# Optimization experiments

Measured on AMD Instinct MI355X. Metric: run time of the kernel, lower is better.

Reference implementation:

```python
import jax, jax.numpy as jnp
import numpy as np

DECAY = 0.85          # decay_factor
LAM = 0.5             # lambda_diversity
EPS = 1e-12


def setup_inputs() -> dict:
    key = jax.random.key(0)
    ks = jax.random.split(key, 6)
    N, D = 32768, 512
    return {
        "predictions": jax.random.normal(ks[0], (N,), jnp.float32),
        "target_scores": jax.random.normal(ks[1], (N,), jnp.float32),
        "context_embeddings": jax.random.normal(ks[2], (N, D), jnp.float32),
        "input_embeddings": jax.random.normal(ks[3], (N, D), jnp.float32),
        "dsm_embeddings": jax.random.normal(ks[4], (N, D), jnp.float32),
        "explanation_embeddings": jax.random.normal(ks[5], (N, D), jnp.float32),
        "k": 16,
    }


def reference(predictions, target_scores, context_embeddings, input_embeddings,
              dsm_embeddings, explanation_embeddings, k):
    # relevance probabilities over all N candidates (dim=0 softmax as in torch)
    rel = jax.nn.softmax(predictions.squeeze(), axis=0)

    # L2-normalize once so cos_sim is a plain dot product
    E = explanation_embeddings
    En = E / (jnp.linalg.norm(E, axis=-1, keepdims=True) + EPS)  # [N, D]
    N = En.shape[0]

    # Greedy ERR/MMR relevance-diversity selection of k items:
    #   score_t(i) = decay^t * rel[i] - lambda * max_{j in selected} cos(E_i, E_j)
    # pick argmax over unselected; err_score_t = decay^t * rel[selected_t]
    def step(carry, t):
        mask, max_sim = carry                       # [N] bool, [N] f32
        decay = DECAY ** t.astype(rel.dtype)
        score = decay * rel - LAM * max_sim
        score = jnp.where(mask, -jnp.inf, score)
        idx = jnp.argmax(score)
        err = rel[idx] * decay
        sim_new = En @ En[idx]                      # cos sim of all to new pick
        return (mask.at[idx].set(True),
                jnp.maximum(max_sim, sim_new)), (err, idx)

    init = (jnp.zeros((N,), bool), jnp.zeros((N,), rel.dtype))
    _, (errs, sel) = jax.lax.scan(step, init, jnp.arange(k))

    err_loss = -jnp.sum(errs)

    # mmr_loss = -sum_i max_j cos(E_i, E_j) over selected set (self included,
    # exactly as the original code does with util.cos_sim(...).max())
    S = En[sel]                                    # [k, D]
    sims = S @ S.T                                 # [k, k]
    mmr_loss = -jnp.sum(jnp.max(sims, axis=1))

    return err_loss + LAM * mmr_loss
```

## Files before the change

kernel.cpp:

```cpp
#include <hip/hip_runtime.h>
#include <cmath>


#define DECAYF 0.85f
#define LAMF   0.5f
#define EPSF   1e-12f

constexpr int D    = 512;
constexpr int KMAX = 16;
constexpr int NBLK = 256;
constexpr int TPB  = 512;
constexpr int NW   = TPB / 64;
constexpr int RPW  = 16;
constexpr int RPB  = NW * RPW;

using u32 = unsigned int;
using u64 = unsigned long long;

__device__ inline float wsum(float v) {
#pragma unroll
    for (int o = 32; o > 0; o >>= 1) v += __shfl_xor(v, o);
    return v;
}
__device__ inline float wmaxf(float v) {
#pragma unroll
    for (int o = 32; o > 0; o >>= 1) v = fmaxf(v, __shfl_xor(v, o));
    return v;
}
__device__ inline u64 wmax64(u64 v) {
#pragma unroll
    for (int o = 32; o > 0; o >>= 1) {
        u64 w = __shfl_xor(v, o);
        v = (w > v) ? w : v;
    }
    return v;
}
__device__ inline u32 fkey(float f) {
    u32 u = __float_as_uint(f);
    return (u & 0x80000000u) ? ~u : (u | 0x80000000u);
}
__device__ inline u64 poll_slot(u64* p) {
    u64 v = __hip_atomic_load(p, __ATOMIC_RELAXED, __HIP_MEMORY_SCOPE_AGENT);
    while (v == 0ull)
        v = __hip_atomic_load(p, __ATOMIC_RELAXED, __HIP_MEMORY_SCOPE_AGENT);
    return v;
}
__device__ inline void publish(u64* p, u64 v) {
    __hip_atomic_store(p, v, __ATOMIC_RELAXED, __HIP_MEMORY_SCOPE_AGENT);
}

__global__ __launch_bounds__(TPB, 2) void fused_kernel(
        const float* __restrict__ pred,
        const float* __restrict__ E,
        const int*   __restrict__ kptr,
        float* __restrict__ out,
        u64*   __restrict__ sm,
        u64*   __restrict__ part,
        u64*   __restrict__ bcast) {
    const int b = blockIdx.x, tid = threadIdx.x;
    const int wv = tid >> 6, lane = tid & 63;

    __shared__ float pred_s[RPB];
    __shared__ u64   wkey_s[NW];
    __shared__ u64   scan_s[NBLK];
    __shared__ float m_s, S_s;
    __shared__ int   j_s;
    __shared__ int   sel_s[KMAX];
    __shared__ float invsel_s[KMAX];
    __shared__ float rmax_s[KMAX];

    int kk = kptr[0];
    if (kk > KMAX) kk = KMAX;
    if (kk < 0) kk = 0;

    if (tid < RPB) pred_s[tid] = pred[b * RPB + tid];
    __syncthreads();
    if (wv == 0) {
        float p0 = pred_s[lane], p1 = pred_s[lane + 64];
        float mb = wmaxf(fmaxf(p0, p1));
        float sb = wsum(expf(p0 - mb) + expf(p1 - mb));
        if (lane == 0)
            publish(&sm[b], ((u64)__float_as_uint(mb) << 32) | __float_as_uint(sb));
    }
    asm volatile("" ::: "memory");

    const int row0 = b * RPB + wv * RPW;
    float r[RPW][8];
#pragma unroll
    for (int rr = 0; rr < RPW; ++rr) {
        const float4* p = (const float4*)(E + (size_t)(row0 + rr) * D) + 2 * lane;
        float4 a0 = p[0], a1 = p[1];
        r[rr][0] = a0.x; r[rr][1] = a0.y; r[rr][2] = a0.z; r[rr][3] = a0.w;
        r[rr][4] = a1.x; r[rr][5] = a1.y; r[rr][6] = a1.z; r[rr][7] = a1.w;
        float ss = 0.f;
#pragma unroll
        for (int e = 0; e < 8; ++e) ss += r[rr][e] * r[rr][e];
        ss = wsum(ss);
        float inv = 1.f / (sqrtf(ss) + EPSF);
#pragma unroll
        for (int e = 0; e < 8; ++e) r[rr][e] *= inv;
        asm volatile("" : "+v"(r[rr][0]), "+v"(r[rr][1]), "+v"(r[rr][2]), "+v"(r[rr][3]),
                          "+v"(r[rr][4]), "+v"(r[rr][5]), "+v"(r[rr][6]), "+v"(r[rr][7]));
    }

    if (tid < NBLK) scan_s[tid] = poll_slot(&sm[tid]);
    __syncthreads();
    if (wv == 0) {
        u64 v0 = scan_s[lane], v1 = scan_s[lane + 64],
            v2 = scan_s[lane + 128], v3 = scan_s[lane + 192];
        float m0 = __uint_as_float((u32)(v0 >> 32)), m1 = __uint_as_float((u32)(v1 >> 32));
        float m2 = __uint_as_float((u32)(v2 >> 32)), m3 = __uint_as_float((u32)(v3 >> 32));
        float M = wmaxf(fmaxf(fmaxf(m0, m1), fmaxf(m2, m3)));
        float acc = __uint_as_float((u32)(v0 & 0xFFFFFFFFull)) * expf(m0 - M)
                  + __uint_as_float((u32)(v1 & 0xFFFFFFFFull)) * expf(m1 - M)
                  + __uint_as_float((u32)(v2 & 0xFFFFFFFFull)) * expf(m2 - M)
                  + __uint_as_float((u32)(v3 & 0xFFFFFFFFull)) * expf(m3 - M);
        acc = wsum(acc);
        if (lane == 0) { m_s = M; S_s = acc; }
    }
    __syncthreads();
    const float M    = m_s;
    const float Sinv = 1.f / S_s;

    float rel_r[RPW], msim_r[RPW];
#pragma unroll
    for (int rr = 0; rr < RPW; ++rr) {
        rel_r[rr]  = expf(pred_s[wv * RPW + rr] - M) * Sinv;
        msim_r[rr] = 0.f;
    }

    int jprev = -1;
    for (int t = 0; t < KMAX; ++t) {
        if (t >= kk) break;
        const float decay = powf(DECAYF, (float)t);
        if (t > 0) {
            const float4* pj = (const float4*)(E + (size_t)jprev * D) + 2 * lane;
            float4 b0 = pj[0], b1 = pj[1];
            float bj[8] = {b0.x, b0.y, b0.z, b0.w, b1.x, b1.y, b1.z, b1.w};
            float ss = 0.f;
#pragma unroll
            for (int e = 0; e < 8; ++e) ss += bj[e] * bj[e];
            ss = wsum(ss);
            const float js = 1.f / (sqrtf(ss) + EPSF);
#pragma unroll
            for (int e = 0; e < 8; ++e) bj[e] *= js;
#pragma unroll
            for (int rr = 0; rr < RPW; ++rr) {
                float d = 0.f;
#pragma unroll
                for (int e = 0; e < 8; ++e) d += r[rr][e] * bj[e];
                d = wsum(d);
                msim_r[rr] = (row0 + rr == jprev) ? INFINITY
                                                  : fmaxf(msim_r[rr], d);
            }
        }
        u64 best = 0ull;
#pragma unroll
        for (int rr = 0; rr < RPW; ++rr) {
            const float sc = decay * rel_r[rr] - LAMF * msim_r[rr];
            const u64 key = ((u64)fkey(sc) << 32) | (u32)~(u32)(row0 + rr);
            best = (key > best) ? key : best;
        }
        if (lane == 0) wkey_s[wv] = best;
        __syncthreads();
        if (wv == 0) {
            u64 v = (lane < NW) ? wkey_s[lane] : 0ull;
            v = wmax64(v);
            if (lane == 0) publish(&part[t * NBLK + b], v);
        }
        if (b == 0) {
            if (tid < NBLK) scan_s[tid] = poll_slot(&part[t * NBLK + tid]);
            __syncthreads();
            if (wv == 0) {
                u64 v = scan_s[lane];
                u64 w = scan_s[lane + 64];  v = (w > v) ? w : v;
                w = scan_s[lane + 128];     v = (w > v) ? w : v;
                w = scan_s[lane + 192];     v = (w > v) ? w : v;
                v = wmax64(v);
                if (lane == 0) publish(&bcast[t], v);
            }
        }
        if (tid == 0) {
            const int j = (int)~(u32)(poll_slot(&bcast[t]) & 0xFFFFFFFFull);
            j_s = j;
            sel_s[t] = j;
        }
        __syncthreads();
        jprev = j_s;
    }

    if (b == 0) {
        for (int ii = wv; ii < kk; ii += NW) {
            const int si = sel_s[ii];
            const float4* pa = (const float4*)(E + (size_t)si * D) + 2 * lane;
            float4 a0 = pa[0], a1 = pa[1];
            float ss = a0.x*a0.x + a0.y*a0.y + a0.z*a0.z + a0.w*a0.w
                     + a1.x*a1.x + a1.y*a1.y + a1.z*a1.z + a1.w*a1.w;
            ss = wsum(ss);
            if (lane == 0) invsel_s[ii] = 1.f / (sqrtf(ss) + EPSF);
        }
        __syncthreads();
        for (int ii = wv; ii < kk; ii += NW) {
            const int si = sel_s[ii];
            const float4* pa = (const float4*)(E + (size_t)si * D) + 2 * lane;
            float4 a0 = pa[0], a1 = pa[1];
            const float ia = invsel_s[ii];
            float av[8] = {a0.x * ia, a0.y * ia, a0.z * ia, a0.w * ia,
                           a1.x * ia, a1.y * ia, a1.z * ia, a1.w * ia};
            float m = -INFINITY;
            for (int jj = 0; jj < kk; ++jj) {
                const float4* pb = (const float4*)(E + (size_t)sel_s[jj] * D) + 2 * lane;
                float4 c0 = pb[0], c1 = pb[1];
                float d = av[0]*c0.x + av[1]*c0.y + av[2]*c0.z + av[3]*c0.w
                        + av[4]*c1.x + av[5]*c1.y + av[6]*c1.z + av[7]*c1.w;
                d = wsum(d);
                m = fmaxf(m, d * invsel_s[jj]);
            }
            if (lane == 0) rmax_s[ii] = m;
        }
        __syncthreads();
        if (tid == 0) {
            float es = 0.f, mm = 0.f;
            for (int t = 0; t < kk; ++t) {
                es += powf(DECAYF, (float)t) * expf(pred[sel_s[t]] - M) * Sinv;
                mm += rmax_s[t];
            }
            out[0] = -es - LAMF * mm;
        }
    }
}

extern "C" void kernel_launch(void* const* d_in, const int* in_sizes, int n_in,
                              void* d_out, int out_size, void* d_ws, size_t ws_size,
                              hipStream_t stream) {
    const float* pred = (const float*)d_in[0];
    const float* E    = (const float*)d_in[5];
    const int*   kptr = (const int*)d_in[6];
    float* out        = (float*)d_out;

    u64* sm    = (u64*)d_ws;
    u64* part  = sm + NBLK;
    u64* bcast = part + KMAX * NBLK;
    hipMemsetAsync(d_ws, 0, (NBLK + KMAX * NBLK + KMAX) * sizeof(u64), stream);

    void* args[] = {(void*)&pred, (void*)&E, (void*)&kptr, (void*)&out,
                    (void*)&sm, (void*)&part, (void*)&bcast};
    hipLaunchCooperativeKernel((const void*)fused_kernel,
                               dim3(NBLK), dim3(TPB), args, 0, stream);
}
```

Before: 156.8 us.

## Replace per-step block barriers with LDS flag polling and widen blocks

Removes the __syncthreads barriers inside the greedy selection loop. Wave 0 instead polls per-step LDS slots for the other waves' keys, does the cross-block reduction (block 0) and the broadcast poll, then publishes the chosen index through an LDS flag that the other waves spin on. Block size doubles to 1024 threads with 8 rows per wave, so each wave keeps fewer rows in registers. An s_sleep is added to the global polling loop to ease memory traffic. The changes add spin-wait risk and alter occupancy and register pressure.

Measured after the change: 161.8 us. 3.2% more time.

```diff
diff --git a/kernel.cpp b/kernel.cpp
--- a/kernel.cpp
+++ b/kernel.cpp
@@ -9,9 +9,9 @@
 constexpr int D    = 512;
 constexpr int KMAX = 16;
 constexpr int NBLK = 256;
-constexpr int TPB  = 512;
+constexpr int TPB  = 1024;
 constexpr int NW   = TPB / 64;
-constexpr int RPW  = 16;
+constexpr int RPW  = 8;
 constexpr int RPB  = NW * RPW;
 
 using u32 = unsigned int;
@@ -41,15 +41,35 @@
 }
 __device__ inline u64 poll_slot(u64* p) {
     u64 v = __hip_atomic_load(p, __ATOMIC_RELAXED, __HIP_MEMORY_SCOPE_AGENT);
-    while (v == 0ull)
+    while (v == 0ull) {
+        __builtin_amdgcn_s_sleep(1);
         v = __hip_atomic_load(p, __ATOMIC_RELAXED, __HIP_MEMORY_SCOPE_AGENT);
+    }
     return v;
 }
 __device__ inline void publish(u64* p, u64 v) {
     __hip_atomic_store(p, v, __ATOMIC_RELAXED, __HIP_MEMORY_SCOPE_AGENT);
 }
-
-__global__ __launch_bounds__(TPB, 2) void fused_kernel(
+__device__ inline u64 lds_poll64(u64* p) {
+    u64 v = __hip_atomic_load(p, __ATOMIC_RELAXED, __HIP_MEMORY_SCOPE_WORKGROUP);
+    while (v == 0ull)
+        v = __hip_atomic_load(p, __ATOMIC_RELAXED, __HIP_MEMORY_SCOPE_WORKGROUP);
+    return v;
+}
+__device__ inline int lds_poll32(int* p) {
+    int v = __hip_atomic_load(p, __ATOMIC_RELAXED, __HIP_MEMORY_SCOPE_WORKGROUP);
+    while (v == 0)
+        v = __hip_atomic_load(p, __ATOMIC_RELAXED, __HIP_MEMORY_SCOPE_WORKGROUP);
+    return v;
+}
+__device__ inline void lds_store64(u64* p, u64 v) {
+    __hip_atomic_store(p, v, __ATOMIC_RELAXED, __HIP_MEMORY_SCOPE_WORKGROUP);
+}
+__device__ inline void lds_store32(int* p, int v) {
+    __hip_atomic_store(p, v, __ATOMIC_RELAXED, __HIP_MEMORY_SCOPE_WORKGROUP);
+}
+
+__global__ __launch_bounds__(TPB, 4) void fused_kernel(
         const float* __restrict__ pred,
         const float* __restrict__ E,
         const int*   __restrict__ kptr,
@@ -61,17 +81,19 @@
     const int wv = tid >> 6, lane = tid & 63;
 
     __shared__ float pred_s[RPB];
-    __shared__ u64   wkey_s[NW];
     __shared__ u64   scan_s[NBLK];
+    __shared__ u64   wkey_s[KMAX][NW];
+    __shared__ int   jslot_s[KMAX];
     __shared__ float m_s, S_s;
-    __shared__ int   j_s;
-    __shared__ int   sel_s[KMAX];
     __shared__ float invsel_s[KMAX];
     __shared__ float rmax_s[KMAX];
 
     int kk = kptr[0];
     if (kk > KMAX) kk = KMAX;
     if (kk < 0) kk = 0;
+
+    if (tid < KMAX) jslot_s[tid] = 0;
+    if (tid < KMAX * NW) ((u64*)wkey_s)[tid] = 0ull;
 
     if (tid < RPB) pred_s[tid] = pred[b * RPB + tid];
     __syncthreads();
@@ -129,12 +151,14 @@
         msim_r[rr] = 0.f;
     }
 
-    int jprev = -1;
+    int j = -1;
     for (int t = 0; t < KMAX; ++t) {
         if (t >= kk) break;
+        if (t > 0 && wv != 0)
+            j = lds_poll32(&jslot_s[t - 1]) - 1;
         const float decay = powf(DECAYF, (float)t);
         if (t > 0) {
-            const float4* pj = (const float4*)(E + (size_t)jprev * D) + 2 * lane;
+            const float4* pj = (const float4*)(E + (size_t)j * D) + 2 * lane;
             float4 b0 = pj[0], b1 = pj[1];
             float bj[8] = {b0.x, b0.y, b0.z, b0.w, b1.x, b1.y, b1.z, b1.w};
             float ss = 0.f;
@@ -150,8 +174,8 @@
 #pragma unroll
                 for (int e = 0; e < 8; ++e) d += r[rr][e] * bj[e];
                 d = wsum(d);
-                msim_r[rr] = (row0 + rr == jprev) ? INFINITY
-                                                  : fmaxf(msim_r[rr], d);
+                msim_r[rr] = (row0 + rr == j) ? INFINITY
+                                              : fmaxf(msim_r[rr], d);
             }
         }
         u64 best = 0ull;
@@ -161,37 +185,36 @@
             const u64 key = ((u64)fkey(sc) << 32) | (u32)~(u32)(row0 + rr);
             best = (key > best) ? key : best;
         }
-        if (lane == 0) wkey_s[wv] = best;
-        __syncthreads();
+        if (lane == 0) lds_store64(&wkey_s[t][wv], best);
+
         if (wv == 0) {
-            u64 v = (lane < NW) ? wkey_s[lane] : 0ull;
+            u64 v = 0ull;
+            if (lane < NW) v = lds_poll64(&wkey_s[t][lane]);
             v = wmax64(v);
             if (lane == 0) publish(&part[t * NBLK + b], v);
-        }
-        if (b == 0) {
-            if (tid < NBLK) scan_s[tid] = poll_slot(&part[t * NBLK + tid]);
-            __syncthreads();
-            if (wv == 0) {
-                u64 v = scan_s[lane];
-                u64 w = scan_s[lane + 64];  v = (w > v) ? w : v;
-                w = scan_s[lane + 128];     v = (w > v) ? w : v;
-                w = scan_s[lane + 192];     v = (w > v) ? w : v;
-                v = wmax64(v);
-                if (lane == 0) publish(&bcast[t], v);
-            }
-        }
-        if (tid == 0) {
-            const int j = (int)~(u32)(poll_slot(&bcast[t]) & 0xFFFFFFFFull);
-            j_s = j;
-            sel_s[t] = j;
-        }
-        __syncthreads();
-        jprev = j_s;
+            if (b == 0) {
+                u64 a0 = poll_slot(&part[t * NBLK + lane]);
+                u64 a1 = poll_slot(&part[t * NBLK + lane + 64]);
+                u64 a2 = poll_slot(&part[t * NBLK + lane + 128]);
+                u64 a3 = poll_slot(&part[t * NBLK + lane + 192]);
+                u64 m = (a1 > a0) ? a1 : a0;
+                m = (a2 > m) ? a2 : m;
+                m = (a3 > m) ? a3 : m;
+                m = wmax64(m);
+                if (lane == 0) publish(&bcast[t], m);
+            }
+            int jj = 0;
+            if (lane == 0) {
+                jj = (int)~(u32)(poll_slot(&bcast[t]) & 0xFFFFFFFFull);
+                lds_store32(&jslot_s[t], jj + 1);
+            }
+            j = __shfl(jj, 0);
+        }
     }
 
     if (b == 0) {
         for (int ii = wv; ii < kk; ii += NW) {
-            const int si = sel_s[ii];
+            const int si = lds_poll32(&jslot_s[ii]) - 1;
             const float4* pa = (const float4*)(E + (size_t)si * D) + 2 * lane;
             float4 a0 = pa[0], a1 = pa[1];
             float ss = a0.x*a0.x + a0.y*a0.y + a0.z*a0.z + a0.w*a0.w
@@ -201,20 +224,21 @@
         }
         __syncthreads();
         for (int ii = wv; ii < kk; ii += NW) {
-            const int si = sel_s[ii];
+            const int si = jslot_s[ii] - 1;
             const float4* pa = (const float4*)(E + (size_t)si * D) + 2 * lane;
             float4 a0 = pa[0], a1 = pa[1];
             const float ia = invsel_s[ii];
             float av[8] = {a0.x * ia, a0.y * ia, a0.z * ia, a0.w * ia,
                            a1.x * ia, a1.y * ia, a1.z * ia, a1.w * ia};
             float m = -INFINITY;
-            for (int jj = 0; jj < kk; ++jj) {
-                const float4* pb = (const float4*)(E + (size_t)sel_s[jj] * D) + 2 * lane;
+            for (int jj2 = 0; jj2 < kk; ++jj2) {
+                const int sj = jslot_s[jj2] - 1;
+                const float4* pb = (const float4*)(E + (size_t)sj * D) + 2 * lane;
                 float4 c0 = pb[0], c1 = pb[1];
                 float d = av[0]*c0.x + av[1]*c0.y + av[2]*c0.z + av[3]*c0.w
                         + av[4]*c1.x + av[5]*c1.y + av[6]*c1.z + av[7]*c1.w;
                 d = wsum(d);
-                m = fmaxf(m, d * invsel_s[jj]);
+                m = fmaxf(m, d * invsel_s[jj2]);
             }
             if (lane == 0) rmax_s[ii] = m;
         }
@@ -222,7 +246,7 @@
         if (tid == 0) {
             float es = 0.f, mm = 0.f;
             for (int t = 0; t < kk; ++t) {
-                es += powf(DECAYF, (float)t) * expf(pred[sel_s[t]] - M) * Sinv;
+                es += powf(DECAYF, (float)t) * expf(pred[jslot_s[t] - 1] - M) * Sinv;
                 mm += rmax_s[t];
             }
             out[0] = -es - LAMF * mm;
```

## Replace single-block reduce-and-broadcast with all-block redundant argmax reduction

Applied to the files above, without the earlier changes.

Each block now polls all per-block partial argmax keys itself and reduces them locally, removing the block-0 reduction stage and the separate broadcast slot, so each step needs one global round trip instead of two. Block size doubles to 1024 threads with half the rows per wave, giving more waves to hide latency, and polling loops add a short sleep to cut memory contention. The decay power is replaced by a running product. This costs 256x more polling reads of the partials array and higher register pressure limits from the new launch bounds.

New measurement: 164.5 us. 1.05x slower.

```diff
diff --git a/kernel.cpp b/kernel.cpp
--- a/kernel.cpp
+++ b/kernel.cpp
@@ -9,9 +9,9 @@
 constexpr int D    = 512;
 constexpr int KMAX = 16;
 constexpr int NBLK = 256;
-constexpr int TPB  = 512;
+constexpr int TPB  = 1024;
 constexpr int NW   = TPB / 64;
-constexpr int RPW  = 16;
+constexpr int RPW  = 8;
 constexpr int RPB  = NW * RPW;
 
 using u32 = unsigned int;
@@ -41,28 +41,29 @@
 }
 __device__ inline u64 poll_slot(u64* p) {
     u64 v = __hip_atomic_load(p, __ATOMIC_RELAXED, __HIP_MEMORY_SCOPE_AGENT);
-    while (v == 0ull)
+    while (v == 0ull) {
+        __builtin_amdgcn_s_sleep(1);
         v = __hip_atomic_load(p, __ATOMIC_RELAXED, __HIP_MEMORY_SCOPE_AGENT);
+    }
     return v;
 }
 __device__ inline void publish(u64* p, u64 v) {
     __hip_atomic_store(p, v, __ATOMIC_RELAXED, __HIP_MEMORY_SCOPE_AGENT);
 }
 
-__global__ __launch_bounds__(TPB, 2) void fused_kernel(
+__global__ __launch_bounds__(TPB, 4) void fused_kernel(
         const float* __restrict__ pred,
         const float* __restrict__ E,
         const int*   __restrict__ kptr,
         float* __restrict__ out,
         u64*   __restrict__ sm,
-        u64*   __restrict__ part,
-        u64*   __restrict__ bcast) {
+        u64*   __restrict__ part) {
     const int b = blockIdx.x, tid = threadIdx.x;
     const int wv = tid >> 6, lane = tid & 63;
 
     __shared__ float pred_s[RPB];
+    __shared__ u64   scan_s[NBLK];
     __shared__ u64   wkey_s[NW];
-    __shared__ u64   scan_s[NBLK];
     __shared__ float m_s, S_s;
     __shared__ int   j_s;
     __shared__ int   sel_s[KMAX];
@@ -122,19 +123,18 @@
     const float M    = m_s;
     const float Sinv = 1.f / S_s;
 
-    float rel_r[RPW], msim_r[RPW];
+    float drel_r[RPW], msim_r[RPW];
 #pragma unroll
     for (int rr = 0; rr < RPW; ++rr) {
-        rel_r[rr]  = expf(pred_s[wv * RPW + rr] - M) * Sinv;
+        drel_r[rr] = expf(pred_s[wv * RPW + rr] - M) * Sinv;
         msim_r[rr] = 0.f;
     }
 
-    int jprev = -1;
+    int j = -1;
     for (int t = 0; t < KMAX; ++t) {
         if (t >= kk) break;
-        const float decay = powf(DECAYF, (float)t);
         if (t > 0) {
-            const float4* pj = (const float4*)(E + (size_t)jprev * D) + 2 * lane;
+            const float4* pj = (const float4*)(E + (size_t)j * D) + 2 * lane;
             float4 b0 = pj[0], b1 = pj[1];
             float bj[8] = {b0.x, b0.y, b0.z, b0.w, b1.x, b1.y, b1.z, b1.w};
             float ss = 0.f;
@@ -150,43 +150,41 @@
 #pragma unroll
                 for (int e = 0; e < 8; ++e) d += r[rr][e] * bj[e];
                 d = wsum(d);
-                msim_r[rr] = (row0 + rr == jprev) ? INFINITY
-                                                  : fmaxf(msim_r[rr], d);
+                msim_r[rr] = (row0 + rr == j) ? INFINITY
+                                              : fmaxf(msim_r[rr], d);
             }
         }
         u64 best = 0ull;
 #pragma unroll
         for (int rr = 0; rr < RPW; ++rr) {
-            const float sc = decay * rel_r[rr] - LAMF * msim_r[rr];
+            const float sc = drel_r[rr] - LAMF * msim_r[rr];
             const u64 key = ((u64)fkey(sc) << 32) | (u32)~(u32)(row0 + rr);
             best = (key > best) ? key : best;
         }
+#pragma unroll
+        for (int rr = 0; rr < RPW; ++rr) drel_r[rr] *= DECAYF;
         if (lane == 0) wkey_s[wv] = best;
         __syncthreads();
         if (wv == 0) {
             u64 v = (lane < NW) ? wkey_s[lane] : 0ull;
             v = wmax64(v);
             if (lane == 0) publish(&part[t * NBLK + b], v);
-        }
-        if (b == 0) {
-            if (tid < NBLK) scan_s[tid] = poll_slot(&part[t * NBLK + tid]);
-            __syncthreads();
-            if (wv == 0) {
-                u64 v = scan_s[lane];
-                u64 w = scan_s[lane + 64];  v = (w > v) ? w : v;
-                w = scan_s[lane + 128];     v = (w > v) ? w : v;
-                w = scan_s[lane + 192];     v = (w > v) ? w : v;
-                v = wmax64(v);
-                if (lane == 0) publish(&bcast[t], v);
-            }
-        }
-        if (tid == 0) {
-            const int j = (int)~(u32)(poll_slot(&bcast[t]) & 0xFFFFFFFFull);
-            j_s = j;
-            sel_s[t] = j;
-        }
-        __syncthreads();
-        jprev = j_s;
+            u64 a0 = poll_slot(&part[t * NBLK + lane]);
+            u64 a1 = poll_slot(&part[t * NBLK + lane + 64]);
+            u64 a2 = poll_slot(&part[t * NBLK + lane + 128]);
+            u64 a3 = poll_slot(&part[t * NBLK + lane + 192]);
+            u64 m = (a1 > a0) ? a1 : a0;
+            m = (a2 > m) ? a2 : m;
+            m = (a3 > m) ? a3 : m;
+            m = wmax64(m);
+            if (lane == 0) {
+                const int jj = (int)~(u32)(m & 0xFFFFFFFFull);
+                j_s = jj;
+                sel_s[t] = jj;
+            }
+        }
+        __syncthreads();
+        j = j_s;
     }
 
     if (b == 0) {
@@ -238,13 +236,12 @@
     const int*   kptr = (const int*)d_in[6];
     float* out        = (float*)d_out;
 
-    u64* sm    = (u64*)d_ws;
-    u64* part  = sm + NBLK;
-    u64* bcast = part + KMAX * NBLK;
-    hipMemsetAsync(d_ws, 0, (NBLK + KMAX * NBLK + KMAX) * sizeof(u64), stream);
+    u64* sm   = (u64*)d_ws;
+    u64* part = sm + NBLK;
+    hipMemsetAsync(d_ws, 0, (NBLK + KMAX * NBLK) * sizeof(u64), stream);
 
     void* args[] = {(void*)&pred, (void*)&E, (void*)&kptr, (void*)&out,
-                    (void*)&sm, (void*)&part, (void*)&bcast};
+                    (void*)&sm, (void*)&part};
     hipLaunchCooperativeKernel((const void*)fused_kernel,
                                dim3(NBLK), dim3(TPB), args, 0, stream);
 }
```
